# Performance work log

Measured on AMD Instinct MI355X. Metric: run time of the kernel, lower is better.

## Reference

```python
import jax, jax.numpy as jnp
import numpy as np

B, C_IN, C_OUT, T = 128, 256, 512, 200
H, K = 8, 64
KS, DIL = 3, 2
PAD = (KS - 1) * DIL  # causal left padding


def setup_inputs() -> dict:
    key = jax.random.key(0)
    ks = jax.random.split(key, 14)
    s = 0.02
    return {
        "x": jax.random.normal(ks[0], (B, C_IN, T), jnp.float32),
        "Wq": jax.random.normal(ks[1], (C_IN, H * K), jnp.float32) * s,
        "bq": jnp.zeros((H * K,), jnp.float32),
        "Wk": jax.random.normal(ks[2], (C_IN, H * K), jnp.float32) * s,
        "bk": jnp.zeros((H * K,), jnp.float32),
        "Wv": jax.random.normal(ks[3], (C_IN, H * C_IN), jnp.float32) * s,
        "bv": jnp.zeros((H * C_IN,), jnp.float32),
        "Wp": jax.random.normal(ks[4], (H * C_IN, C_IN), jnp.float32) * s,
        "bp": jnp.zeros((C_IN,), jnp.float32),
        "Wc": jax.random.normal(ks[5], (C_OUT, C_IN, KS), jnp.float32) * s,
        "bc": jnp.zeros((C_OUT,), jnp.float32),
        "Wd": jax.random.normal(ks[6], (C_OUT, C_IN, 1), jnp.float32) * s,
        "bd": jnp.zeros((C_OUT,), jnp.float32),
    }


def reference(x, Wq, bq, Wk, bk, Wv, bv, Wp, bp, Wc, bc, Wd, bd):
    xp = jnp.transpose(x, (0, 2, 1))  # (B,T,C)
    q = (xp @ Wq + bq).reshape(B, T, H, K).transpose(0, 2, 1, 3)       # (B,H,T,K)
    k = (xp @ Wk + bk).reshape(B, T, H, K).transpose(0, 2, 1, 3)       # (B,H,T,K)
    v = (xp @ Wv + bv).reshape(B, T, H, C_IN).transpose(0, 2, 1, 3)    # (B,H,T,C)
    scores = jnp.einsum("bhtk,bhsk->bhts", q, k) / np.sqrt(K).astype(jnp.float32)
    mask = jnp.tril(jnp.ones((T, T), bool))
    scores = jnp.where(mask, scores, -jnp.inf)
    att = jax.nn.softmax(scores, axis=-1)                               # (B,H,T,T)
    y = jnp.einsum("bhts,bhsc->bhtc", att, v)                           # (B,H,T,C)
    y = y.transpose(0, 2, 1, 3).reshape(B, T, H * C_IN)
    attn_out = (y @ Wp + bp).transpose(0, 2, 1)                         # (B,C,T)
    conv = jax.lax.conv_general_dilated(
        attn_out, Wc, window_strides=(1,), padding=[(PAD, 0)],
        rhs_dilation=(DIL,), dimension_numbers=("NCH", "OIH", "NCH"))
    conv = jax.nn.relu(conv + bc[None, :, None])                        # (B,C_OUT,T)
    res = jnp.einsum("oi,bit->bot", Wd[:, :, 0], x) + bd[None, :, None]
    return jax.nn.relu(conv + res), att
```

## Files before the change

### kernel.cpp

```cpp
#include <hip/hip_runtime.h>
#include <hip/hip_bf16.h>
#include <math.h>

#define BB 128
#define CIN 256
#define COUT 512
#define TT 200
#define HH 8
#define KD 64
#define HK 512
#define HC 2048
#define QR 56

typedef __hip_bfloat16 bf16;
typedef __attribute__((ext_vector_type(8))) short s16x8;
typedef __attribute__((ext_vector_type(4))) short s16x4;
typedef __attribute__((ext_vector_type(4))) float f32x4;

#define MFMA(a, b, c) __builtin_amdgcn_mfma_f32_16x16x32_bf16(a, b, c, 0, 0, 0)

__device__ __forceinline__ short bfs(float f) {
  bf16 h = __float2bfloat16(f);
  return *reinterpret_cast<short*>(&h);
}
__device__ __forceinline__ s16x8 ld8(const bf16* p) {
  return *reinterpret_cast<const s16x8*>(p);
}

__global__ __launch_bounds__(256) void k_xb(const float* __restrict__ x, bf16* __restrict__ xb,
                                            bf16* __restrict__ xtb) {
  __shared__ float lx[CIN][33];
  int blk = blockIdx.x, b = blk / 7, tt = blk % 7, t0 = tt * 32;
  int tid = threadIdx.x;
  const float* xbp = x + (size_t)b * CIN * TT;
  bf16* xo = xb + (size_t)b * 208 * CIN;
  bf16* xto = xtb + (size_t)b * CIN * 224;
  for (int idx = tid; idx < CIN * 32; idx += 256) {
    int c = idx >> 5, tl = idx & 31, t = t0 + tl;
    lx[c][tl] = (t < TT) ? xbp[(size_t)c * TT + t] : 0.f;
  }
  __syncthreads();
  for (int idx = tid; idx < CIN * 32; idx += 256) {
    int c = idx >> 5, tl = idx & 31;
    xto[(size_t)c * 224 + t0 + tl] = __float2bfloat16(lx[c][tl]);
  }
  for (int idx = tid; idx < 32 * 64; idx += 256) {
    int tl = idx >> 6, cs = idx & 63, t = t0 + tl;
    if (t < TT) {
      s16x4 p;
      p[0] = bfs(lx[cs * 4 + 0][tl]); p[1] = bfs(lx[cs * 4 + 1][tl]);
      p[2] = bfs(lx[cs * 4 + 2][tl]); p[3] = bfs(lx[cs * 4 + 3][tl]);
      *reinterpret_cast<s16x4*>(&xo[(size_t)t * CIN + cs * 4]) = p;
    }
  }
  if (tt == 6) {
    s16x4 z = {0, 0, 0, 0};
    for (int idx = tid; idx < 8 * 64; idx += 256) {
      int r = 200 + (idx >> 6), cs = idx & 63;
      *reinterpret_cast<s16x4*>(&xo[(size_t)r * CIN + cs * 4]) = z;
    }
  }
}

__global__ __launch_bounds__(256) void k_wc(const float* __restrict__ Wc,
    const float* __restrict__ Wd, bf16* __restrict__ Wcb, bf16* __restrict__ Wdb) {
  int o = blockIdx.x, i = threadIdx.x;
  size_t oi = (size_t)o * CIN + i;
#pragma unroll
  for (int j = 0; j < 3; ++j)
    Wcb[(size_t)j * COUT * CIN + oi] = __float2bfloat16(Wc[oi * 3 + j]);
  Wdb[oi] = __float2bfloat16(Wd[oi]);
}

__global__ __launch_bounds__(256) void k_wqk(const float* __restrict__ Wq,
    const float* __restrict__ Wk, bf16* __restrict__ WqT, bf16* __restrict__ WkT) {
  int n = blockIdx.x, ci = threadIdx.x;
  WqT[(size_t)n * CIN + ci] = __float2bfloat16(Wq[(size_t)ci * HK + n]);
  WkT[(size_t)n * CIN + ci] = __float2bfloat16(Wk[(size_t)ci * HK + n]);
}

__global__ __launch_bounds__(256) void k_wvp(const float* __restrict__ Wv,
    const float* __restrict__ Wp, const float* __restrict__ bv,
    bf16* __restrict__ WvpT, float* __restrict__ bvp) {
  __shared__ __align__(16) float wpl[32][256];
  __shared__ __align__(16) float wvl[17][32];
  int h = blockIdx.x >> 4, ci0 = (blockIdx.x & 15) << 4;
  int c = threadIdx.x;
  float acc[17];
#pragma unroll
  for (int i = 0; i < 17; ++i) acc[i] = 0.f;
  for (int p0 = 0; p0 < CIN; p0 += 32) {
    __syncthreads();
    for (int idx = c; idx < 17 * 32; idx += 256) {
      int pp = idx & 31, cil = idx >> 5;
      wvl[cil][pp] = (cil < 16) ? Wv[(size_t)(ci0 + cil) * HC + h * CIN + p0 + pp]
                                : bv[h * CIN + p0 + pp];
    }
    for (int idx = c; idx < 32 * 256; idx += 256) {
      int cc = idx & 255, pp = idx >> 8;
      wpl[pp][cc] = Wp[(size_t)(h * CIN + p0 + pp) * CIN + cc];
    }
    __syncthreads();
#pragma unroll 4
    for (int pp = 0; pp < 32; ++pp) {
      float w = wpl[pp][c];
#pragma unroll
      for (int i = 0; i < 17; ++i) acc[i] += wvl[i][pp] * w;
    }
  }
  for (int i = 0; i < 16; ++i)
    WvpT[((size_t)h * CIN + c) * CIN + ci0 + i] = __float2bfloat16(acc[i]);
  if (ci0 == 0) bvp[h * CIN + c] = acc[16];
}

__global__ __launch_bounds__(256) void k_qk(const bf16* __restrict__ xb,
    const bf16* __restrict__ WqT, const bf16* __restrict__ WkT,
    const float* __restrict__ bq, const float* __restrict__ bk,
    bf16* __restrict__ qo, bf16* __restrict__ kvo) {
  int blk = blockIdx.x, b = blk & 127, quad = blk >> 7;
  int tid = threadIdx.x, w = tid >> 6, l = tid & 63;
  int lrow = l & 15, g = l >> 4;
  int cw = quad * 64 + w * 16 + lrow;
  const bf16* xbb = xb + (size_t)b * 208 * CIN;
  const bf16* wqt = WqT + (size_t)cw * CIN;
  const bf16* wkt = WkT + (size_t)cw * CIN;
  f32x4 aq[13], ak[13];
#pragma unroll
  for (int mt = 0; mt < 13; ++mt) {
    aq[mt] = (f32x4){0.f, 0.f, 0.f, 0.f};
    ak[mt] = (f32x4){0.f, 0.f, 0.f, 0.f};
  }
  for (int kc = 0; kc < 8; ++kc) {
    int kof = kc * 32 + g * 8;
    s16x8 bqf = ld8(&wqt[kof]);
    s16x8 bkf = ld8(&wkt[kof]);
#pragma unroll
    for (int mt = 0; mt < 13; ++mt) {
      s16x8 afr = ld8(&xbb[(size_t)(mt * 16 + lrow) * CIN + kof]);
      aq[mt] = MFMA(afr, bqf, aq[mt]);
      ak[mt] = MFMA(afr, bkf, ak[mt]);
    }
  }
  float bqv = bq[cw], bkv = bk[cw];
#pragma unroll
  for (int mt = 0; mt < 13; ++mt) {
#pragma unroll
    for (int r = 0; r < 4; ++r) {
      int t = mt * 16 + g * 4 + r;
      if (t < TT) {
        qo[((size_t)b * TT + t) * HK + cw] = __float2bfloat16(aq[mt][r] + bqv);
        kvo[((size_t)b * TT + t) * HK + cw] = __float2bfloat16(ak[mt][r] + bkv);
      }
    }
  }
}

__global__ __launch_bounds__(256) void k_attn(const bf16* __restrict__ qo,
    const bf16* __restrict__ kvo, float* __restrict__ att) {
  int bh = blockIdx.x, b = bh >> 3, h = bh & 7;
  int tid = threadIdx.x, w = tid >> 6, l = tid & 63;
  int lrow = l & 15, g = l >> 4;
  const bf16* qb = qo + (size_t)b * TT * HK + h * KD;
  const bf16* kb = kvo + (size_t)b * TT * HK + h * KD;
  float* ab = att + (size_t)bh * TT * TT;
  for (int mt = w; mt < 13; mt += 4) {
    int ra = mt * 16 + lrow; if (ra > TT - 1) ra = TT - 1;
    s16x8 a0 = ld8(&qb[(size_t)ra * HK + g * 8]);
    s16x8 a1 = ld8(&qb[(size_t)ra * HK + 32 + g * 8]);
    f32x4 sacc[13];
#pragma unroll
    for (int st = 0; st < 13; ++st) sacc[st] = (f32x4){0.f, 0.f, 0.f, 0.f};
#pragma unroll
    for (int st = 0; st < 13; ++st) {
      if (st <= mt) {
        int rb = st * 16 + lrow; if (rb > TT - 1) rb = TT - 1;
        s16x8 b0 = ld8(&kb[(size_t)rb * HK + g * 8]);
        s16x8 b1 = ld8(&kb[(size_t)rb * HK + 32 + g * 8]);
        sacc[st] = MFMA(a0, b0, sacc[st]);
        sacc[st] = MFMA(a1, b1, sacc[st]);
      }
    }
#pragma unroll
    for (int r = 0; r < 4; ++r) {
      int m = mt * 16 + g * 4 + r;
      if (m >= TT) continue;
      float vals[13];
      float mx = -INFINITY;
#pragma unroll
      for (int st = 0; st < 13; ++st) {
        int col = st * 16 + lrow;
        float v = sacc[st][r] * 0.125f;
        vals[st] = (st <= mt && col <= m) ? v : -INFINITY;
        mx = fmaxf(mx, vals[st]);
      }
#pragma unroll
      for (int off = 1; off < 16; off <<= 1) mx = fmaxf(mx, __shfl_xor(mx, off));
      float e[13], sum = 0.f;
#pragma unroll
      for (int st = 0; st < 13; ++st) {
        e[st] = (vals[st] > -INFINITY) ? __expf(vals[st] - mx) : 0.f;
        sum += e[st];
      }
#pragma unroll
      for (int off = 1; off < 16; off <<= 1) sum += __shfl_xor(sum, off);
      float inv = 1.f / sum;
#pragma unroll
      for (int st = 0; st < 13; ++st) {
        int col = st * 16 + lrow;
        if (col < TT) ab[(size_t)m * TT + col] = e[st] * inv;
      }
    }
  }
}

__global__ __launch_bounds__(512) void k_avx(const float* __restrict__ att,
    const bf16* __restrict__ xtb, const bf16* __restrict__ WvpT,
    const float* __restrict__ bvp, const float* __restrict__ bp,
    bf16* __restrict__ atTp) {
  __shared__ short satt[64 * 232];
  __shared__ short yl[64 * 260];
  int blk = blockIdx.x, b = blk & 127, q = blk >> 7;
  int t0 = q * QR;
  int tid = threadIdx.x, w = tid >> 6, l = tid & 63;
  int lrow = l & 15, g = l >> 4;
  bf16* atb = atTp + (size_t)b * 216 * CIN;
  bf16 zb = __float2bfloat16(0.f);
  if (q == 0) { for (int idx = tid; idx < 4 * CIN; idx += 512) atb[idx] = zb; }
  if (q == 3) { for (int idx = tid; idx < 8 * CIN; idx += 512) atb[204 * CIN + idx] = zb; }
  const bf16* xr = xtb + (size_t)b * CIN * 224;
  int ns = (t0 + QR - 1) / 32 + 1; if (ns > 7) ns = 7;
  f32x4 acc2[4][2];
#pragma unroll
  for (int mt = 0; mt < 4; ++mt)
#pragma unroll
    for (int nt = 0; nt < 2; ++nt) acc2[mt][nt] = (f32x4){0.f, 0.f, 0.f, 0.f};
  for (int h = 0; h < HH; ++h) {
    const float* abh = att + (size_t)(b * HH + h) * TT * TT;
    __syncthreads();
    int nchunk = ns * 8;
    for (int idx = tid; idx < 64 * nchunk; idx += 512) {
      int row = idx / nchunk, ch = idx % nchunk;
      int sra = t0 + row; if (sra > TT - 1) sra = TT - 1;
      int col = ch * 4;
      float4 v = {0.f, 0.f, 0.f, 0.f};
      if (col < TT) v = *(const float4*)&abh[(size_t)sra * TT + col];
      s16x4 p;
      p[0] = bfs(v.x); p[1] = bfs(v.y); p[2] = bfs(v.z); p[3] = bfs(v.w);
      *reinterpret_cast<s16x4*>(&satt[row * 232 + ch * 4]) = p;
    }
    __syncthreads();
    f32x4 acc1[2][4];
#pragma unroll
    for (int mc = 0; mc < 2; ++mc)
#pragma unroll
      for (int nt = 0; nt < 4; ++nt) acc1[mc][nt] = (f32x4){0.f, 0.f, 0.f, 0.f};
    for (int s0 = 0; s0 < ns * 32; s0 += 32) {
      s16x8 bat[4];
#pragma unroll
      for (int nt = 0; nt < 4; ++nt)
        bat[nt] = *reinterpret_cast<const s16x8*>(&satt[(nt * 16 + lrow) * 232 + s0 + g * 8]);
#pragma unroll
      for (int mc = 0; mc < 2; ++mc) {
        s16x8 af = ld8(&xr[(size_t)(w * 32 + mc * 16 + lrow) * 224 + s0 + g * 8]);
#pragma unroll
        for (int nt = 0; nt < 4; ++nt)
          acc1[mc][nt] = MFMA(af, bat[nt], acc1[mc][nt]);
      }
    }
    __syncthreads();
#pragma unroll
    for (int mc = 0; mc < 2; ++mc)
#pragma unroll
      for (int nt = 0; nt < 4; ++nt) {
        s16x4 p;
        p[0] = bfs(acc1[mc][nt][0]); p[1] = bfs(acc1[mc][nt][1]);
        p[2] = bfs(acc1[mc][nt][2]); p[3] = bfs(acc1[mc][nt][3]);
        *reinterpret_cast<s16x4*>(&yl[(nt * 16 + lrow) * 260 + w * 32 + mc * 16 + g * 4]) = p;
      }
    __syncthreads();
    const bf16* wv = WvpT + (size_t)h * CIN * CIN;
#pragma unroll
    for (int kc = 0; kc < 8; ++kc) {
      int kof = kc * 32 + g * 8;
      s16x8 bw[2];
#pragma unroll
      for (int nt = 0; nt < 2; ++nt)
        bw[nt] = ld8(&wv[(size_t)(w * 32 + nt * 16 + lrow) * CIN + kof]);
#pragma unroll
      for (int mt = 0; mt < 4; ++mt) {
        s16x4 alo = *reinterpret_cast<const s16x4*>(&yl[(mt * 16 + lrow) * 260 + kof]);
        s16x4 ahi = *reinterpret_cast<const s16x4*>(&yl[(mt * 16 + lrow) * 260 + kof + 4]);
        s16x8 ay;
        ay[0] = alo[0]; ay[1] = alo[1]; ay[2] = alo[2]; ay[3] = alo[3];
        ay[4] = ahi[0]; ay[5] = ahi[1]; ay[6] = ahi[2]; ay[7] = ahi[3];
#pragma unroll
        for (int nt = 0; nt < 2; ++nt)
          acc2[mt][nt] = MFMA(ay, bw[nt], acc2[mt][nt]);
      }
    }
  }
  int climit = TT - t0; if (climit > QR) climit = QR;
#pragma unroll
  for (int nt = 0; nt < 2; ++nt) {
    int c = w * 32 + nt * 16 + lrow;
    float bsum = bp[c];
#pragma unroll
    for (int h = 0; h < HH; ++h) bsum += bvp[h * CIN + c];
#pragma unroll
    for (int mt = 0; mt < 4; ++mt) {
#pragma unroll
      for (int r = 0; r < 4; ++r) {
        int tloc = mt * 16 + g * 4 + r;
        if (tloc < climit)
          atb[(size_t)(t0 + tloc + 4) * CIN + c] = __float2bfloat16(acc2[mt][nt][r] + bsum);
      }
    }
  }
}

__global__ __launch_bounds__(256) void k_conv(const bf16* __restrict__ atTp,
    const bf16* __restrict__ xb, const bf16* __restrict__ Wcb, const bf16* __restrict__ Wdb,
    const float* __restrict__ bc, const float* __restrict__ bd, float* __restrict__ out0) {
  __shared__ short satb[116 * 64];
  __shared__ short sxb[112 * 64];
  int blk = blockIdx.x, b = blk & 127, og = (blk >> 7) & 7, th = blk >> 10;
  int t0 = th * 100;
  int tid = threadIdx.x, w = tid >> 6, l = tid & 63;
  int lrow = l & 15, g = l >> 4;
  int o0 = og * 64 + w * 16;
  const bf16* wc0 = Wcb + (size_t)(o0 + lrow) * CIN;
  const bf16* wc1 = wc0 + (size_t)COUT * CIN;
  const bf16* wc2 = wc1 + (size_t)COUT * CIN;
  const bf16* wdp = Wdb + (size_t)(o0 + lrow) * CIN;
  const bf16* atb = atTp + (size_t)b * 216 * CIN;
  const bf16* xbb = xb + (size_t)b * 208 * CIN;
  f32x4 accc[7], accr[7];
#pragma unroll
  for (int nt = 0; nt < 7; ++nt) {
    accc[nt] = (f32x4){0.f, 0.f, 0.f, 0.f};
    accr[nt] = (f32x4){0.f, 0.f, 0.f, 0.f};
  }
  for (int ks = 0; ks < 4; ++ks) {
    int kb0 = ks * 64;
    __syncthreads();
    for (int idx = tid; idx < 116 * 8; idx += 256) {
      int row = idx >> 3, ch = idx & 7;
      s16x8 v = ld8(&atb[(size_t)(t0 + row) * CIN + kb0 + ch * 8]);
      *reinterpret_cast<s16x8*>(&satb[row * 64 + ((ch ^ (row & 7)) * 8)]) = v;
    }
    for (int idx = tid; idx < 112 * 8; idx += 256) {
      int row = idx >> 3, ch = idx & 7;
      int grow = t0 + row; if (grow > 207) grow = 207;
      s16x8 v = ld8(&xbb[(size_t)grow * CIN + kb0 + ch * 8]);
      *reinterpret_cast<s16x8*>(&sxb[row * 64 + ((ch ^ (row & 7)) * 8)]) = v;
    }
    __syncthreads();
#pragma unroll
    for (int kcl = 0; kcl < 2; ++kcl) {
      int kof = kb0 + kcl * 32 + g * 8;
      s16x8 a0 = ld8(&wc0[kof]);
      s16x8 a1 = ld8(&wc1[kof]);
      s16x8 a2 = ld8(&wc2[kof]);
      s16x8 ad = ld8(&wdp[kof]);
      int chb = kcl * 4 + g;
#pragma unroll
      for (int nt = 0; nt < 7; ++nt) {
        int r0 = nt * 16 + lrow, r1 = r0 + 2, r2 = r0 + 4;
        s16x8 b0 = *reinterpret_cast<const s16x8*>(&satb[r0 * 64 + ((chb ^ (r0 & 7)) * 8)]);
        s16x8 b1 = *reinterpret_cast<const s16x8*>(&satb[r1 * 64 + ((chb ^ (r1 & 7)) * 8)]);
        s16x8 b2 = *reinterpret_cast<const s16x8*>(&satb[r2 * 64 + ((chb ^ (r2 & 7)) * 8)]);
        s16x8 bx = *reinterpret_cast<const s16x8*>(&sxb[r0 * 64 + ((chb ^ (r0 & 7)) * 8)]);
        accc[nt] = MFMA(a0, b0, accc[nt]);
        accc[nt] = MFMA(a1, b1, accc[nt]);
        accc[nt] = MFMA(a2, b2, accc[nt]);
        accr[nt] = MFMA(ad, bx, accr[nt]);
      }
    }
  }
  f32x4 bcv = *reinterpret_cast<const f32x4*>(&bc[o0 + g * 4]);
  f32x4 bdv = *reinterpret_cast<const f32x4*>(&bd[o0 + g * 4]);
#pragma unroll
  for (int nt = 0; nt < 7; ++nt) {
    int tloc = nt * 16 + lrow;
    if (tloc < 100) {
      int t = t0 + tloc;
#pragma unroll
      for (int r = 0; r < 4; ++r) {
        int o = o0 + g * 4 + r;
        float conv = fmaxf(accc[nt][r] + bcv[r], 0.f);
        out0[((size_t)b * COUT + o) * TT + t] = fmaxf(conv + accr[nt][r] + bdv[r], 0.f);
      }
    }
  }
}

extern "C" void kernel_launch(void* const* d_in, const int* in_sizes, int n_in,
                              void* d_out, int out_size, void* d_ws, size_t ws_size,
                              hipStream_t stream) {
  const float* x  = (const float*)d_in[0];
  const float* Wq = (const float*)d_in[1];
  const float* bq = (const float*)d_in[2];
  const float* Wk = (const float*)d_in[3];
  const float* bk = (const float*)d_in[4];
  const float* Wv = (const float*)d_in[5];
  const float* bv = (const float*)d_in[6];
  const float* Wp = (const float*)d_in[7];
  const float* bp = (const float*)d_in[8];
  const float* Wc = (const float*)d_in[9];
  const float* bc = (const float*)d_in[10];
  const float* Wd = (const float*)d_in[11];
  const float* bd = (const float*)d_in[12];

  float* out0 = (float*)d_out;
  float* att  = out0 + (size_t)BB * COUT * TT;

  char* ws = (char*)d_ws;
  bf16*  qo   = (bf16*)(ws);
  bf16*  atTp = (bf16*)(ws);
  bf16*  kvo  = (bf16*)(ws + 26214400);
  bf16*  xtb  = (bf16*)(ws + 52428800);
  bf16*  xb   = (bf16*)(ws + 157286400);
  bf16*  WvpT = (bf16*)(ws + 170917888);
  float* bvp  = (float*)(ws + 171966464);
  bf16*  Wcb  = (bf16*)(ws + 171974656);
  bf16*  Wdb  = (bf16*)(ws + 172761088);
  bf16*  WqT  = (bf16*)(ws + 173023232);
  bf16*  WkT  = (bf16*)(ws + 173285376);

  hipLaunchKernelGGL(k_wvp,  dim3(128),      dim3(256), 0, stream, Wv, Wp, bv, WvpT, bvp);
  hipLaunchKernelGGL(k_wc,   dim3(COUT),     dim3(256), 0, stream, Wc, Wd, Wcb, Wdb);
  hipLaunchKernelGGL(k_wqk,  dim3(HK),       dim3(256), 0, stream, Wq, Wk, WqT, WkT);
  hipLaunchKernelGGL(k_xb,   dim3(BB * 7),   dim3(256), 0, stream, x, xb, xtb);
  hipLaunchKernelGGL(k_qk,   dim3(BB * 8),   dim3(256), 0, stream, xb, WqT, WkT, bq, bk, qo, kvo);
  hipLaunchKernelGGL(k_attn, dim3(BB * HH),  dim3(256), 0, stream, qo, kvo, att);
  hipLaunchKernelGGL(k_avx,  dim3(BB * 4),   dim3(512), 0, stream, att, xtb, WvpT, bvp, bp, atTp);
  hipLaunchKernelGGL(k_conv, dim3(BB * 16),  dim3(256), 0, stream, atTp, xb, Wcb, Wdb, bc, bd, out0);
}
```

Before: 383.3 us.

## Register-prefetch next tile loads in attention-V and conv kernels

```diff
diff --git a/kernel.cpp b/kernel.cpp
--- a/kernel.cpp
+++ b/kernel.cpp
@@ -229,24 +229,55 @@
   if (q == 3) { for (int idx = tid; idx < 8 * CIN; idx += 512) atb[204 * CIN + idx] = zb; }
   const bf16* xr = xtb + (size_t)b * CIN * 224;
   int ns = (t0 + QR - 1) / 32 + 1; if (ns > 7) ns = 7;
+  int nchunk = ns * 8;
+  int tot = 64 * nchunk;
+  float4 pre[7];
+  {
+    const float* abh0 = att + (size_t)(b * HH) * TT * TT;
+#pragma unroll
+    for (int j = 0; j < 7; ++j) {
+      pre[j] = (float4){0.f, 0.f, 0.f, 0.f};
+      int idx = tid + j * 512;
+      if (idx < tot) {
+        int row = idx / nchunk, ch = idx - row * nchunk;
+        int sra = t0 + row; if (sra > TT - 1) sra = TT - 1;
+        int col = ch * 4;
+        if (col < TT) pre[j] = *(const float4*)&att[(size_t)(b * HH) * TT * TT + (size_t)sra * TT + col];
+        (void)abh0;
+      }
+    }
+  }
   f32x4 acc2[4][2];
 #pragma unroll
   for (int mt = 0; mt < 4; ++mt)
 #pragma unroll
     for (int nt = 0; nt < 2; ++nt) acc2[mt][nt] = (f32x4){0.f, 0.f, 0.f, 0.f};
   for (int h = 0; h < HH; ++h) {
-    const float* abh = att + (size_t)(b * HH + h) * TT * TT;
-    __syncthreads();
-    int nchunk = ns * 8;
-    for (int idx = tid; idx < 64 * nchunk; idx += 512) {
-      int row = idx / nchunk, ch = idx % nchunk;
-      int sra = t0 + row; if (sra > TT - 1) sra = TT - 1;
-      int col = ch * 4;
-      float4 v = {0.f, 0.f, 0.f, 0.f};
-      if (col < TT) v = *(const float4*)&abh[(size_t)sra * TT + col];
-      s16x4 p;
-      p[0] = bfs(v.x); p[1] = bfs(v.y); p[2] = bfs(v.z); p[3] = bfs(v.w);
-      *reinterpret_cast<s16x4*>(&satt[row * 232 + ch * 4]) = p;
+    __syncthreads();
+#pragma unroll
+    for (int j = 0; j < 7; ++j) {
+      int idx = tid + j * 512;
+      if (idx < tot) {
+        int row = idx / nchunk, ch = idx - row * nchunk;
+        s16x4 p;
+        p[0] = bfs(pre[j].x); p[1] = bfs(pre[j].y); p[2] = bfs(pre[j].z); p[3] = bfs(pre[j].w);
+        *reinterpret_cast<s16x4*>(&satt[row * 232 + ch * 4]) = p;
+      }
+    }
+    if (h < HH - 1) {
+      const float* abn = att + (size_t)(b * HH + h + 1) * TT * TT;
+#pragma unroll
+      for (int j = 0; j < 7; ++j) {
+        int idx = tid + j * 512;
+        if (idx < tot) {
+          int row = idx / nchunk, ch = idx - row * nchunk;
+          int sra = t0 + row; if (sra > TT - 1) sra = TT - 1;
+          int col = ch * 4;
+          float4 v = {0.f, 0.f, 0.f, 0.f};
+          if (col < TT) v = *(const float4*)&abn[(size_t)sra * TT + col];
+          pre[j] = v;
+        }
+      }
     }
     __syncthreads();
     f32x4 acc1[2][4];
@@ -340,19 +371,44 @@
     accc[nt] = (f32x4){0.f, 0.f, 0.f, 0.f};
     accr[nt] = (f32x4){0.f, 0.f, 0.f, 0.f};
   }
+  s16x8 pa[4], px[4];
+  const s16x8 z8 = {0, 0, 0, 0, 0, 0, 0, 0};
+#pragma unroll
+  for (int j = 0; j < 4; ++j) {
+    int idx = tid + j * 256;
+    pa[j] = z8; px[j] = z8;
+    if (idx < 116 * 8) pa[j] = ld8(&atb[(size_t)(t0 + (idx >> 3)) * CIN + (idx & 7) * 8]);
+    if (idx < 112 * 8) {
+      int gx = t0 + (idx >> 3); if (gx > 207) gx = 207;
+      px[j] = ld8(&xbb[(size_t)gx * CIN + (idx & 7) * 8]);
+    }
+  }
   for (int ks = 0; ks < 4; ++ks) {
     int kb0 = ks * 64;
     __syncthreads();
-    for (int idx = tid; idx < 116 * 8; idx += 256) {
-      int row = idx >> 3, ch = idx & 7;
-      s16x8 v = ld8(&atb[(size_t)(t0 + row) * CIN + kb0 + ch * 8]);
-      *reinterpret_cast<s16x8*>(&satb[row * 64 + ((ch ^ (row & 7)) * 8)]) = v;
-    }
-    for (int idx = tid; idx < 112 * 8; idx += 256) {
-      int row = idx >> 3, ch = idx & 7;
-      int grow = t0 + row; if (grow > 207) grow = 207;
-      s16x8 v = ld8(&xbb[(size_t)grow * CIN + kb0 + ch * 8]);
-      *reinterpret_cast<s16x8*>(&sxb[row * 64 + ((ch ^ (row & 7)) * 8)]) = v;
+#pragma unroll
+    for (int j = 0; j < 4; ++j) {
+      int idx = tid + j * 256;
+      if (idx < 116 * 8) {
+        int row = idx >> 3, ch = idx & 7;
+        *reinterpret_cast<s16x8*>(&satb[row * 64 + ((ch ^ (row & 7)) * 8)]) = pa[j];
+      }
+      if (idx < 112 * 8) {
+        int row = idx >> 3, ch = idx & 7;
+        *reinterpret_cast<s16x8*>(&sxb[row * 64 + ((ch ^ (row & 7)) * 8)]) = px[j];
+      }
+    }
+    if (ks < 3) {
+      int kb1 = kb0 + 64;
+#pragma unroll
+      for (int j = 0; j < 4; ++j) {
+        int idx = tid + j * 256;
+        if (idx < 116 * 8) pa[j] = ld8(&atb[(size_t)(t0 + (idx >> 3)) * CIN + kb1 + (idx & 7) * 8]);
+        if (idx < 112 * 8) {
+          int gx = t0 + (idx >> 3); if (gx > 207) gx = 207;
+          px[j] = ld8(&xbb[(size_t)gx * CIN + kb1 + (idx & 7) * 8]);
+        }
+      }
     }
     __syncthreads();
 #pragma unroll
```

After: 387.2 us. No clear change (+1.0%).
